# Kernel optimization log

Measured on AMD Instinct MI355X. Metric: run time of the kernel, lower is better.

The kernel has to match this reference:

```python
import jax, jax.numpy as jnp
import numpy as np

N = 100000   # node_num / batch_node_num (full-graph batch, identity remap)
E = 600000   # edges in adj[nodes, :]
D_IN = 128
D_OUT = 128
MASK = (1.0, 1.0, 0.0, 0.0)  # self-loop mask per `ind` in original forward


def setup_inputs() -> dict:
    key = jax.random.key(0)
    ks = jax.random.split(key, 6)
    feat = jax.random.normal(ks[0], (N, D_IN), dtype=jnp.float32)
    edge_src = jax.random.randint(ks[1], (E,), 0, N)
    edge_dst = jax.random.randint(ks[2], (E,), 0, N)
    W_edge = jax.random.uniform(ks[3], (E,), dtype=jnp.float32)  # W[u][v] per edge
    W1 = jax.random.normal(ks[4], (D_IN, D_OUT), dtype=jnp.float32) / np.sqrt(D_IN).astype(np.float32)
    b1 = jnp.zeros((D_OUT,), jnp.float32)
    W2 = jax.random.normal(ks[5], (D_OUT, D_OUT), dtype=jnp.float32) / np.sqrt(D_OUT).astype(np.float32)
    b2 = jnp.zeros((D_OUT,), jnp.float32)
    return {"feat": feat, "W_edge": W_edge, "W1": W1, "b1": b1, "W2": W2,
            "b2": b2, "edge_src": edge_src, "edge_dst": edge_dst, "ind": 2}


def reference(feat, W_edge, W1, b1, W2, b2, edge_src, edge_dst, ind):
    # values: self-loop edges get mask[ind], others 1 (torch.where on edges[:,0]==edges[:,1])
    mask_val = MASK[ind]  # ind is a static Python int
    values = jnp.where(edge_src == edge_dst, jnp.float32(mask_val), jnp.float32(1.0))
    # degree[v] = row-sum of matrix_coo (spmm with ones); temp_e = degree[dst_e]
    degree = jax.ops.segment_sum(values, edge_src, num_segments=N)
    # new_embeddings = Linear -> Tanh -> Linear on features of (all) unique nodes
    h = jnp.tanh(feat @ W1 + b1) @ W2 + b2  # [N, D_OUT]
    # matrix = matrix_neighbor .* matrix_weight -> per-edge weight degree[dst]*W[u][v]
    w = degree[edge_dst] * W_edge  # [E]
    # results = spmm(matrix, new_embeddings); row_sum = spmm(matrix, ones)
    results = jax.ops.segment_sum(w[:, None] * h[edge_dst], edge_src, num_segments=N)
    row_sum = jax.ops.segment_sum(w, edge_src, num_segments=N)
    row_sum = jnp.where(row_sum == 0, jnp.float32(1.0), row_sum)
    return results / row_sum[:, None]
```

## Files before the change

kernel.cpp:

```cpp
#include <hip/hip_runtime.h>


constexpr int D = 128;
constexpr int MAXDEG = 24;
constexpr int OVF_CAP = 131072;

typedef __attribute__((ext_vector_type(8))) short short8;
typedef __attribute__((ext_vector_type(4))) float f32x4;
struct ushort8_s { unsigned short v[8]; };

__device__ __forceinline__ unsigned short f2bf(float x) {
    unsigned int u = __float_as_uint(x);
    u += 0x7fffu + ((u >> 16) & 1u);
    return (unsigned short)(u >> 16);
}
__device__ __forceinline__ float bflo(unsigned int u) { return __uint_as_float(u << 16); }
__device__ __forceinline__ float bfhi(unsigned int u) { return __uint_as_float(u & 0xffff0000u); }
__device__ __forceinline__ float fast_tanh(float x) {
    float e = exp2f(x * 2.885390081777927f);
    return fmaf(-2.0f, __builtin_amdgcn_rcpf(e + 1.0f), 1.0f);
}
__device__ __forceinline__ int swz(int row, int kbyte) {
    return (row * 256 + kbyte) ^ ((row & 7) << 4);
}

__global__ __launch_bounds__(256) void k_init(const float* __restrict__ W1,
                                              const float* __restrict__ W2,
                                              unsigned short* __restrict__ Wt1s,
                                              unsigned short* __restrict__ Wt2s,
                                              int* __restrict__ zbase, int zv4) {
    int b = blockIdx.x;
    if (b < 64) {
        int t = b * 256 + threadIdx.x;
        int k = t >> 7, nn = t & 127;
        int si = swz(nn, k * 2) >> 1;
        Wt1s[si] = f2bf(W1[t]);
        Wt2s[si] = f2bf(W2[t]);
    } else {
        int i = (b - 64) * 256 + threadIdx.x;
        if (i < zv4) ((int4*)zbase)[i] = make_int4(0, 0, 0, 0);
    }
}

__global__ __launch_bounds__(512, 4) void k_mlp_place(
        const float* __restrict__ feat,
        const unsigned short* __restrict__ Wt1s,
        const unsigned short* __restrict__ Wt2s,
        const float* __restrict__ b1, const float* __restrict__ b2,
        unsigned short* __restrict__ hbf, int n, int nm, int npl,
        const int* __restrict__ src, const int* __restrict__ dst,
        const float* __restrict__ W_edge,
        unsigned int* __restrict__ packed,
        int* __restrict__ ovf_cnt, int4* __restrict__ ovf,
        float2* __restrict__ pairs, int E) {
    __shared__ unsigned short sW1[128 * D];
    __shared__ unsigned short sW2[128 * D];

    const int bid = blockIdx.x;
    bool isMlp;
    int idx;
    if (nm <= npl) {
        if (bid < 2 * nm) { isMlp = !(bid & 1); idx = bid >> 1; }
        else { isMlp = false; idx = nm + (bid - 2 * nm); }
    } else {
        if (bid < 2 * npl) { isMlp = (bid & 1); idx = bid >> 1; }
        else { isMlp = true; idx = npl + (bid - 2 * npl); }
    }

    if (!isMlp) {
        int e0 = idx * 2048 + threadIdx.x;
#pragma unroll
        for (int q = 0; q < 4; ++q) {
            int e = e0 + q * 512;
            if (e < E) {
                int s = src[e];
                int d = dst[e];
                float W = W_edge[e];
                unsigned int add = (s == d) ? 0x10001u : 1u;
                unsigned int old = atomicAdd(&packed[s], add);
                int rank = (int)(old & 0xffffu);
                if (rank < MAXDEG) {
                    float2 p;
                    p.x = __int_as_float(d);
                    p.y = W;
                    pairs[(size_t)s * MAXDEG + rank] = p;
                } else {
                    int oi = atomicAdd(ovf_cnt, 1);
                    if (oi < OVF_CAP) ovf[oi] = make_int4(s, d, __float_as_int(W), 0);
                }
            }
        }
        return;
    }
    const int t = threadIdx.x;
    const int lane = t & 63;
    const int w = t >> 6;
    const int rl0 = w * 16;
    const int row0 = idx * 128 + rl0;
    const int rA = lane & 15;
    const int ks = (lane >> 4) * 8;

    float4 f[4][2];
    {
        int gr = row0 + rA;
        bool ok = gr < n;
        const float* fp = &feat[(size_t)(ok ? gr : 0) * D + ks];
#pragma unroll
        for (int kc = 0; kc < 4; ++kc) {
            f[kc][0] = ok ? *(const float4*)(fp + kc * 32) : make_float4(0.f, 0.f, 0.f, 0.f);
            f[kc][1] = ok ? *(const float4*)(fp + kc * 32 + 4) : make_float4(0.f, 0.f, 0.f, 0.f);
        }
    }

    {
        const ushort8_s* g1 = (const ushort8_s*)Wt1s;
        const ushort8_s* g2 = (const ushort8_s*)Wt2s;
        ushort8_s* l1 = (ushort8_s*)sW1;
        ushort8_s* l2 = (ushort8_s*)sW2;
#pragma unroll
        for (int j = 0; j < 4; ++j) {
            int c = t + j * 512;
            l1[c] = g1[c];
            l2[c] = g2[c];
        }
    }

    float bias1[8], bias2[8];
#pragma unroll
    for (int nf = 0; nf < 8; ++nf) {
        bias1[nf] = b1[nf * 16 + rA];
        bias2[nf] = b2[nf * 16 + rA];
    }

    short8 afrag[4];
#pragma unroll
    for (int kc = 0; kc < 4; ++kc) {
        float4 f0 = f[kc][0], f1 = f[kc][1];
        short8 a;
        a[0] = (short)f2bf(f0.x); a[1] = (short)f2bf(f0.y);
        a[2] = (short)f2bf(f0.z); a[3] = (short)f2bf(f0.w);
        a[4] = (short)f2bf(f1.x); a[5] = (short)f2bf(f1.y);
        a[6] = (short)f2bf(f1.z); a[7] = (short)f2bf(f1.w);
        afrag[kc] = a;
    }

    __syncthreads();

    f32x4 acc[8];
#pragma unroll
    for (int nf = 0; nf < 8; ++nf) acc[nf] = (f32x4){0.f, 0.f, 0.f, 0.f};

#pragma unroll
    for (int kc = 0; kc < 4; ++kc) {
        const int kb = (kc * 32 + ks) * 2;
#pragma unroll
        for (int nf = 0; nf < 8; ++nf) {
            const int rb = nf * 16 + rA;
            short8 b = *(short8*)((char*)sW1 + swz(rb, kb));
            acc[nf] = __builtin_amdgcn_mfma_f32_16x16x32_bf16(afrag[kc], b, acc[nf], 0, 0, 0);
        }
    }

    __syncthreads();

#pragma unroll
    for (int nf = 0; nf < 8; ++nf) {
        const int col = nf * 16 + rA;
#pragma unroll
        for (int i = 0; i < 4; ++i) {
            const int rl = rl0 + (lane >> 4) * 4 + i;
            unsigned short hv = f2bf(fast_tanh(acc[nf][i] + bias1[nf]));
            *(unsigned short*)((char*)sW1 + swz(rl, col * 2)) = hv;
        }
    }

#pragma unroll
    for (int nf = 0; nf < 8; ++nf) acc[nf] = (f32x4){0.f, 0.f, 0.f, 0.f};

#pragma unroll
    for (int kc = 0; kc < 4; ++kc) {
        const int kb = (kc * 32 + ks) * 2;
        const int ra0 = rl0 + rA;
        short8 a0 = *(short8*)((char*)sW1 + swz(ra0, kb));
#pragma unroll
        for (int nf = 0; nf < 8; ++nf) {
            const int rb = nf * 16 + rA;
            short8 b = *(short8*)((char*)sW2 + swz(rb, kb));
            acc[nf] = __builtin_amdgcn_mfma_f32_16x16x32_bf16(a0, b, acc[nf], 0, 0, 0);
        }
    }

#pragma unroll
    for (int nf = 0; nf < 8; ++nf) {
        const int col = nf * 16 + rA;
#pragma unroll
        for (int i = 0; i < 4; ++i) {
            const int rl = rl0 + (lane >> 4) * 4 + i;
            unsigned short hv = f2bf(acc[nf][i] + bias2[nf]);
            *(unsigned short*)((char*)sW1 + swz(rl, col * 2)) = hv;
        }
    }

    for (int c = lane; c < 256; c += 64) {
        int r = c >> 4, k0 = (c & 15) * 8;
        int gr = row0 + r;
        if (gr < n) {
            int rl = rl0 + r;
            short8 v = *(short8*)((char*)sW1 + swz(rl, k0 * 2));
            *(short8*)&hbf[(size_t)gr * D + k0] = v;
        }
    }
}

__global__ __launch_bounds__(256) void k_aggregate(const unsigned int* __restrict__ packed,
                                                   const float2* __restrict__ pairs,
                                                   const int* __restrict__ ovf_cnt,
                                                   const int4* __restrict__ ovf,
                                                   const unsigned short* __restrict__ hbf,
                                                   const int* __restrict__ indp,
                                                   float* __restrict__ out, int n, int ngroups) {
    const int li = threadIdx.x & 15;
    const int lane = threadIdx.x & 63;
    const int gbase = lane & 48;
    const int group = (int)(((long long)blockIdx.x * 256 + threadIdx.x) >> 4);
    const float maskm1 = ((indp[0] < 2) ? 1.0f : 0.0f) - 1.0f;
    int ovn = *ovf_cnt;
    if (ovn > OVF_CAP) ovn = OVF_CAP;

    float acc[8];
    auto fma8 = [&acc](float w, uint4 h) {
        acc[0] = fmaf(w, bflo(h.x), acc[0]); acc[1] = fmaf(w, bfhi(h.x), acc[1]);
        acc[2] = fmaf(w, bflo(h.y), acc[2]); acc[3] = fmaf(w, bfhi(h.y), acc[3]);
        acc[4] = fmaf(w, bflo(h.z), acc[4]); acc[5] = fmaf(w, bfhi(h.z), acc[5]);
        acc[6] = fmaf(w, bflo(h.w), acc[6]); acc[7] = fmaf(w, bfhi(h.w), acc[7]);
    };

    int mtA = 0;
    float2 pvA = make_float2(0.f, 0.f);
    float wvA = 0.f;
    if (group < n) {
        unsigned int c = packed[group];
        mtA = (int)(c & 0xffffu);
        mtA = (mtA < MAXDEG) ? mtA : MAXDEG;
        pvA = pairs[(size_t)group * MAXDEG + li];
        int lim = (mtA < 16) ? mtA : 16;
        if (li < lim) {
            int d = __float_as_int(pvA.x);
            unsigned int pkd = packed[d];
            float deg = (float)(pkd & 0xffffu) + maskm1 * (float)(pkd >> 16);
            wvA = deg * pvA.y;
        }
    }

    for (int node = group; node < n; node += ngroups) {
        int nxt = node + ngroups;
        int mtB = 0;
        float2 pvB = make_float2(0.f, 0.f);
        float wvB = 0.f;
        if (nxt < n) {
            unsigned int c = packed[nxt];
            mtB = (int)(c & 0xffffu);
            mtB = (mtB < MAXDEG) ? mtB : MAXDEG;
            pvB = pairs[(size_t)nxt * MAXDEG + li];
            int lim = (mtB < 16) ? mtB : 16;
            if (li < lim) {
                int d = __float_as_int(pvB.x);
                unsigned int pkd = packed[d];
                float deg = (float)(pkd & 0xffffu) + maskm1 * (float)(pkd >> 16);
                wvB = deg * pvB.y;
            }
        }

#pragma unroll
        for (int j = 0; j < 8; ++j) acc[j] = 0.f;
        float rsp = wvA;
        int mm = (mtA < 16) ? mtA : 16;
        int i = 0;
        for (; i + 3 < mm; i += 4) {
            int d0 = __float_as_int(__shfl(pvA.x, gbase + i));
            float w0 = __shfl(wvA, gbase + i);
            int d1 = __float_as_int(__shfl(pvA.x, gbase + i + 1));
            float w1 = __shfl(wvA, gbase + i + 1);
            int d2 = __float_as_int(__shfl(pvA.x, gbase + i + 2));
            float w2 = __shfl(wvA, gbase + i + 2);
            int d3 = __float_as_int(__shfl(pvA.x, gbase + i + 3));
            float w3 = __shfl(wvA, gbase + i + 3);
            uint4 h0 = *(const uint4*)&hbf[(size_t)d0 * D + li * 8];
            uint4 h1 = *(const uint4*)&hbf[(size_t)d1 * D + li * 8];
            uint4 h2 = *(const uint4*)&hbf[(size_t)d2 * D + li * 8];
            uint4 h3 = *(const uint4*)&hbf[(size_t)d3 * D + li * 8];
            fma8(w0, h0); fma8(w1, h1); fma8(w2, h2); fma8(w3, h3);
        }
        for (; i + 1 < mm; i += 2) {
            int d0 = __float_as_int(__shfl(pvA.x, gbase + i));
            float w0 = __shfl(wvA, gbase + i);
            int d1 = __float_as_int(__shfl(pvA.x, gbase + i + 1));
            float w1 = __shfl(wvA, gbase + i + 1);
            uint4 h0 = *(const uint4*)&hbf[(size_t)d0 * D + li * 8];
            uint4 h1 = *(const uint4*)&hbf[(size_t)d1 * D + li * 8];
            fma8(w0, h0); fma8(w1, h1);
        }
        if (i < mm) {
            int d0 = __float_as_int(__shfl(pvA.x, gbase + i));
            float w0 = __shfl(wvA, gbase + i);
            uint4 h0 = *(const uint4*)&hbf[(size_t)d0 * D + li * 8];
            fma8(w0, h0);
        }

        if (mtA > 16) {
            const float2* prow = &pairs[(size_t)node * MAXDEG];
            int rem = mtA - 16;
            float wv2 = 0.f, dv2 = 0.f;
            if (li < rem) {
                float2 p = prow[16 + li];
                dv2 = p.x;
                int d = __float_as_int(p.x);
                unsigned int pkd = packed[d];
                float deg = (float)(pkd & 0xffffu) + maskm1 * (float)(pkd >> 16);
                wv2 = deg * p.y;
            }
            rsp += wv2;
            for (int i2 = 0; i2 < rem; ++i2) {
                int d0 = __float_as_int(__shfl(dv2, gbase + i2));
                float w0 = __shfl(wv2, gbase + i2);
                uint4 h0 = *(const uint4*)&hbf[(size_t)d0 * D + li * 8];
                fma8(w0, h0);
            }
        }

        if (ovn > 0) {
            for (int k = 0; k < ovn; ++k) {
                int4 tq = ovf[k];
                if (tq.x == node) {
                    int d = tq.y;
                    unsigned int pkd = packed[d];
                    float deg = (float)(pkd & 0xffffu) + maskm1 * (float)(pkd >> 16);
                    float wq = deg * __int_as_float(tq.z);
                    if (li == 0) rsp += wq;
                    uint4 h = *(const uint4*)&hbf[(size_t)d * D + li * 8];
                    fma8(wq, h);
                }
            }
        }

        rsp += __shfl_xor(rsp, 1);
        rsp += __shfl_xor(rsp, 2);
        rsp += __shfl_xor(rsp, 4);
        rsp += __shfl_xor(rsp, 8);
        rsp = (rsp == 0.f) ? 1.f : rsp;
        float inv = 1.0f / rsp;
        float4 o0, o1;
        o0.x = acc[0] * inv; o0.y = acc[1] * inv; o0.z = acc[2] * inv; o0.w = acc[3] * inv;
        o1.x = acc[4] * inv; o1.y = acc[5] * inv; o1.z = acc[6] * inv; o1.w = acc[7] * inv;
        float* op = &out[(size_t)node * D + li * 8];
        *(float4*)op = o0;
        *(float4*)(op + 4) = o1;

        mtA = mtB; pvA = pvB; wvA = wvB;
    }
}

extern "C" void kernel_launch(void* const* d_in, const int* in_sizes, int n_in,
                              void* d_out, int out_size, void* d_ws, size_t ws_size,
                              hipStream_t stream) {
    const float* feat   = (const float*)d_in[0];
    const float* W_edge = (const float*)d_in[1];
    const float* W1     = (const float*)d_in[2];
    const float* b1     = (const float*)d_in[3];
    const float* W2     = (const float*)d_in[4];
    const float* b2     = (const float*)d_in[5];
    const int* edge_src = (const int*)d_in[6];
    const int* edge_dst = (const int*)d_in[7];
    const int* indp     = (const int*)d_in[8];

    const int n = in_sizes[0] / D;
    const int E = in_sizes[6];

    char* ws = (char*)d_ws;
    unsigned short* Wt1s = (unsigned short*)ws;
    unsigned short* Wt2s = Wt1s + D * D;
    unsigned int* packed = (unsigned int*)(Wt2s + D * D);
    int* ovf_cnt         = (int*)(packed + n);
    int4* ovf            = (int4*)((char*)ovf_cnt + 16);
    float2* pairs        = (float2*)(ovf + OVF_CAP);
    unsigned short* hbf  = (unsigned short*)(pairs + (size_t)n * MAXDEG);

    const int zbytes = n * 4 + 16;
    const int zv4 = zbytes / 16;
    const int zb = (zv4 + 255) / 256;
    k_init<<<64 + zb, 256, 0, stream>>>(W1, W2, Wt1s, Wt2s, (int*)packed, zv4);

    const int nm = (n + 127) / 128;
    const int npl = (E + 2047) / 2048;
    k_mlp_place<<<nm + npl, 512, 0, stream>>>(feat, Wt1s, Wt2s, b1, b2, hbf, n, nm, npl,
                                              edge_src, edge_dst, W_edge,
                                              packed, ovf_cnt, ovf, pairs, E);

    const int ab = 2048;
    const int ngroups = ab * 16;
    k_aggregate<<<ab, 256, 0, stream>>>(packed, pairs, ovf_cnt, ovf, hbf, indp,
                                        (float*)d_out, n, ngroups);
}
```

Measured before the change: 97.44 us.

## Fuse edge placement into MLP blocks to hide atomic latency behind matmuls

Removes the separate edge-placement blocks and has every MLP block also place a contiguous slice of edges, up to two per thread. Each block loads its edges and issues the degree atomics early, then runs the MLP, and writes the pair or overflow entries at the end. The aim is to hide atomic and gather latency behind the MLP compute and to cut the launched block count. The cost is more registers held live across the MLP. Edges are silently dropped if the per-block edge count exceeds 1024, which holds only while E is at most about eight times the node count.

```diff
diff --git a/kernel.cpp b/kernel.cpp
--- a/kernel.cpp
+++ b/kernel.cpp
@@ -47,58 +47,31 @@
         const unsigned short* __restrict__ Wt1s,
         const unsigned short* __restrict__ Wt2s,
         const float* __restrict__ b1, const float* __restrict__ b2,
-        unsigned short* __restrict__ hbf, int n, int nm, int npl,
+        unsigned short* __restrict__ hbf, int n,
         const int* __restrict__ src, const int* __restrict__ dst,
         const float* __restrict__ W_edge,
         unsigned int* __restrict__ packed,
         int* __restrict__ ovf_cnt, int4* __restrict__ ovf,
-        float2* __restrict__ pairs, int E) {
+        float2* __restrict__ pairs, int E, int epb) {
     __shared__ unsigned short sW1[128 * D];
     __shared__ unsigned short sW2[128 * D];
-
-    const int bid = blockIdx.x;
-    bool isMlp;
-    int idx;
-    if (nm <= npl) {
-        if (bid < 2 * nm) { isMlp = !(bid & 1); idx = bid >> 1; }
-        else { isMlp = false; idx = nm + (bid - 2 * nm); }
-    } else {
-        if (bid < 2 * npl) { isMlp = (bid & 1); idx = bid >> 1; }
-        else { isMlp = true; idx = npl + (bid - 2 * npl); }
-    }
-
-    if (!isMlp) {
-        int e0 = idx * 2048 + threadIdx.x;
-#pragma unroll
-        for (int q = 0; q < 4; ++q) {
-            int e = e0 + q * 512;
-            if (e < E) {
-                int s = src[e];
-                int d = dst[e];
-                float W = W_edge[e];
-                unsigned int add = (s == d) ? 0x10001u : 1u;
-                unsigned int old = atomicAdd(&packed[s], add);
-                int rank = (int)(old & 0xffffu);
-                if (rank < MAXDEG) {
-                    float2 p;
-                    p.x = __int_as_float(d);
-                    p.y = W;
-                    pairs[(size_t)s * MAXDEG + rank] = p;
-                } else {
-                    int oi = atomicAdd(ovf_cnt, 1);
-                    if (oi < OVF_CAP) ovf[oi] = make_int4(s, d, __float_as_int(W), 0);
-                }
-            }
-        }
-        return;
-    }
     const int t = threadIdx.x;
     const int lane = t & 63;
     const int w = t >> 6;
     const int rl0 = w * 16;
-    const int row0 = idx * 128 + rl0;
+    const int row0 = blockIdx.x * 128 + rl0;
     const int rA = lane & 15;
     const int ks = (lane >> 4) * 8;
+
+    const int ebase = blockIdx.x * epb;
+    const int e1 = ebase + t;
+    const int e2 = e1 + 512;
+    const bool v1 = (t < epb) && (e1 < E);
+    const bool v2 = (t < epb - 512) && (e2 < E);
+    int s1 = 0, d1 = 0, s2 = 0, d2 = 0;
+    float ew1 = 0.f, ew2 = 0.f;
+    if (v1) { s1 = src[e1]; d1 = dst[e1]; ew1 = W_edge[e1]; }
+    if (v2) { s2 = src[e2]; d2 = dst[e2]; ew2 = W_edge[e2]; }
 
     float4 f[4][2];
     {
@@ -124,6 +97,10 @@
             l2[c] = g2[c];
         }
     }
+
+    unsigned int old1 = 0, old2 = 0;
+    if (v1) old1 = atomicAdd(&packed[s1], (s1 == d1) ? 0x10001u : 1u);
+    if (v2) old2 = atomicAdd(&packed[s2], (s2 == d2) ? 0x10001u : 1u);
 
     float bias1[8], bias2[8];
 #pragma unroll
@@ -208,6 +185,31 @@
             int rl = rl0 + r;
             short8 v = *(short8*)((char*)sW1 + swz(rl, k0 * 2));
             *(short8*)&hbf[(size_t)gr * D + k0] = v;
+        }
+    }
+
+    if (v1) {
+        int rank = (int)(old1 & 0xffffu);
+        if (rank < MAXDEG) {
+            float2 p;
+            p.x = __int_as_float(d1);
+            p.y = ew1;
+            pairs[(size_t)s1 * MAXDEG + rank] = p;
+        } else {
+            int oi = atomicAdd(ovf_cnt, 1);
+            if (oi < OVF_CAP) ovf[oi] = make_int4(s1, d1, __float_as_int(ew1), 0);
+        }
+    }
+    if (v2) {
+        int rank = (int)(old2 & 0xffffu);
+        if (rank < MAXDEG) {
+            float2 p;
+            p.x = __int_as_float(d2);
+            p.y = ew2;
+            pairs[(size_t)s2 * MAXDEG + rank] = p;
+        } else {
+            int oi = atomicAdd(ovf_cnt, 1);
+            if (oi < OVF_CAP) ovf[oi] = make_int4(s2, d2, __float_as_int(ew2), 0);
         }
     }
 }
@@ -391,10 +393,10 @@
     k_init<<<64 + zb, 256, 0, stream>>>(W1, W2, Wt1s, Wt2s, (int*)packed, zv4);
 
     const int nm = (n + 127) / 128;
-    const int npl = (E + 2047) / 2048;
-    k_mlp_place<<<nm + npl, 512, 0, stream>>>(feat, Wt1s, Wt2s, b1, b2, hbf, n, nm, npl,
-                                              edge_src, edge_dst, W_edge,
-                                              packed, ovf_cnt, ovf, pairs, E);
+    const int epb = (E + nm - 1) / nm;
+    k_mlp_place<<<nm, 512, 0, stream>>>(feat, Wt1s, Wt2s, b1, b2, hbf, n,
+                                        edge_src, edge_dst, W_edge,
+                                        packed, ovf_cnt, ovf, pairs, E, epb);
 
     const int ab = 2048;
     const int ngroups = ab * 16;
```

Measured after the change: 96.32 us. No clear change (-1.2%).
